# Performance work log

Hardware: AMD Instinct MI355X
Metric: run time of the kernel (lower is better)

The kernel has to match this reference:

```python
import jax, jax.numpy as jnp
import numpy as np


def setup_inputs() -> dict:
    key = jax.random.key(0)
    k1, k2 = jax.random.split(key)
    B, L, D = 32, 1024, 384
    MAX_LEN = 8192
    x = jax.random.normal(k1, (B, L, D), dtype=jnp.float32)
    # float durations in [0, 12); module rounds+clamps internally
    durations = jax.random.uniform(k2, (B, L), dtype=jnp.float32) * 12.0
    return {"x": x, "durations": durations, "max_len": MAX_LEN}


def reference(x, durations, max_len):
    # x: [B, L, D], durations: [B, L] (float), max_len: static python int
    B, L, D = x.shape
    dur = jnp.round(jnp.clip(durations, 0)).astype(jnp.int32)        # [B, L]
    cum = jnp.cumsum(dur, axis=1)                                    # [B, L] exclusive ends
    total = cum[:, -1]                                               # [B] expanded lengths
    t = jnp.arange(max_len, dtype=jnp.int32)                         # [T]
    # frame t belongs to phoneme idx where cum[idx-1] <= t < cum[idx]
    idx = jax.vmap(lambda c: jnp.searchsorted(c, t, side='right'))(cum)  # [B, T]
    idx = jnp.clip(idx, 0, L - 1)
    out = jnp.take_along_axis(x, idx[:, :, None], axis=1)            # [B, T, D]
    mask = (t[None, :] < total[:, None])[:, :, None]                 # [B, T, 1]
    return jnp.where(mask, out, jnp.zeros((), dtype=x.dtype))
```

## Files before the change

kernel.cpp:

```cpp
#include <hip/hip_runtime.h>
#include <hip/hip_bf16.h>


#define L_FIXED 1024
#define TILE_T 128
#define ROW_F4 96

__global__ __launch_bounds__(1024) void lr_cumsum_kernel(
    const float* __restrict__ durations, int* __restrict__ cum, int L) {
    __shared__ int s[L_FIXED];
    const int b = blockIdx.x;
    const int tid = threadIdx.x;
    float d = durations[b * L + tid];
    s[tid] = (int)rintf(fmaxf(d, 0.0f));
    __syncthreads();
#pragma unroll
    for (int off = 1; off < L_FIXED; off <<= 1) {
        int add = (tid >= off) ? s[tid - off] : 0;
        __syncthreads();
        s[tid] += add;
        __syncthreads();
    }
    cum[b * L + tid] = s[tid];
}

__global__ __launch_bounds__(256) void lr_gather_kernel(
    const float4* __restrict__ x, const int* __restrict__ cum,
    float4* __restrict__ out, int L, int max_len) {
    __shared__ int s_cum[L_FIXED];
    __shared__ int s_idx[TILE_T];
    const int b = blockIdx.y;
    const int t0 = blockIdx.x * TILE_T;
    const int tid = threadIdx.x;

    for (int i = tid; i < L; i += 256) s_cum[i] = cum[b * L + i];
    __syncthreads();

    const int total = s_cum[L - 1];
    if (tid < TILE_T) {
        const int t = t0 + tid;
        int lo = 0, hi = L;
        while (lo < hi) {
            int mid = (lo + hi) >> 1;
            if (s_cum[mid] <= t) lo = mid + 1; else hi = mid;
        }
        int idx = min(lo, L - 1);
        s_idx[tid] = (t < total) ? idx : -1;
    }
    __syncthreads();

    const long out_base = ((long)b * max_len + t0) * ROW_F4;
    const long x_base = (long)b * L * ROW_F4;
#pragma unroll
    for (int j = tid; j < TILE_T * ROW_F4; j += 256) {
        const int tl = j / ROW_F4;
        const int c = j - tl * ROW_F4;
        const int row = s_idx[tl];
        float4 v;
        if (row >= 0) {
            v = x[x_base + (long)row * ROW_F4 + c];
        } else {
            v = make_float4(0.f, 0.f, 0.f, 0.f);
        }
        out[out_base + (long)tl * ROW_F4 + c] = v;
    }
}

extern "C" void kernel_launch(void* const* d_in, const int* in_sizes, int n_in,
                              void* d_out, int out_size, void* d_ws, size_t ws_size,
                              hipStream_t stream) {
    const float* x = (const float*)d_in[0];
    const float* durations = (const float*)d_in[1];

    const int B = 32;
    const int L = 1024;
    const int MAX_LEN = 8192;

    int* cum = (int*)d_ws;

    lr_cumsum_kernel<<<B, L_FIXED, 0, stream>>>(durations, cum, L);

    dim3 grid(MAX_LEN / TILE_T, B);
    lr_gather_kernel<<<grid, 256, 0, stream>>>(
        (const float4*)x, cum, (float4*)d_out, L, MAX_LEN);
}
```

Measured before the change: 467.6 us.

## Move index search into scan kernel and use 2D row-copy gather blocks

The binary search from frame to phoneme now runs inside the per-batch scan kernel, which writes a precomputed index array to the workspace. The gather kernel then only loads 32 indices per block and copies rows with a 96x4 thread layout, so no integer division is needed. This removes the redundant per-block loading of the cumsum array and the search from the memory-bound copy. In exchange, the search now runs on only 32 blocks, which serialises it onto few CUs, and the copy grid becomes four times larger with smaller blocks.

```diff
diff --git a/kernel.cpp b/kernel.cpp
--- a/kernel.cpp
+++ b/kernel.cpp
@@ -2,67 +2,59 @@
 #include <hip/hip_bf16.h>
 
 
+#define B_FIXED 32
 #define L_FIXED 1024
-#define TILE_T 128
 #define ROW_F4 96
+#define RPB 32
 
-__global__ __launch_bounds__(1024) void lr_cumsum_kernel(
-    const float* __restrict__ durations, int* __restrict__ cum, int L) {
+__global__ __launch_bounds__(1024) void lr_scan_idx_kernel(
+    const float* __restrict__ durations, int* __restrict__ idx, int max_len) {
     __shared__ int s[L_FIXED];
     const int b = blockIdx.x;
     const int tid = threadIdx.x;
-    float d = durations[b * L + tid];
+    float d = durations[b * L_FIXED + tid];
     s[tid] = (int)rintf(fmaxf(d, 0.0f));
     __syncthreads();
-#pragma unroll
     for (int off = 1; off < L_FIXED; off <<= 1) {
         int add = (tid >= off) ? s[tid - off] : 0;
         __syncthreads();
         s[tid] += add;
         __syncthreads();
     }
-    cum[b * L + tid] = s[tid];
+    const int total = s[L_FIXED - 1];
+    for (int t = tid; t < max_len; t += 1024) {
+        int lo = 0, hi = L_FIXED;
+        while (lo < hi) {
+            int mid = (lo + hi) >> 1;
+            if (s[mid] <= t) lo = mid + 1; else hi = mid;
+        }
+        int v = min(lo, L_FIXED - 1);
+        idx[b * max_len + t] = (t < total) ? v : -1;
+    }
 }
 
-__global__ __launch_bounds__(256) void lr_gather_kernel(
-    const float4* __restrict__ x, const int* __restrict__ cum,
-    float4* __restrict__ out, int L, int max_len) {
-    __shared__ int s_cum[L_FIXED];
-    __shared__ int s_idx[TILE_T];
+__global__ __launch_bounds__(384) void lr_copy_kernel(
+    const float4* __restrict__ x, const int* __restrict__ idx,
+    float4* __restrict__ out, int max_len) {
+    __shared__ int s_idx[RPB];
     const int b = blockIdx.y;
-    const int t0 = blockIdx.x * TILE_T;
-    const int tid = threadIdx.x;
-
-    for (int i = tid; i < L; i += 256) s_cum[i] = cum[b * L + i];
+    const int t0 = blockIdx.x * RPB;
+    const int lin = threadIdx.y * 96 + threadIdx.x;
+    if (lin < RPB) s_idx[lin] = idx[b * max_len + t0 + lin];
     __syncthreads();
 
-    const int total = s_cum[L - 1];
-    if (tid < TILE_T) {
-        const int t = t0 + tid;
-        int lo = 0, hi = L;
-        while (lo < hi) {
-            int mid = (lo + hi) >> 1;
-            if (s_cum[mid] <= t) lo = mid + 1; else hi = mid;
-        }
-        int idx = min(lo, L - 1);
-        s_idx[tid] = (t < total) ? idx : -1;
-    }
-    __syncthreads();
-
-    const long out_base = ((long)b * max_len + t0) * ROW_F4;
-    const long x_base = (long)b * L * ROW_F4;
-#pragma unroll
-    for (int j = tid; j < TILE_T * ROW_F4; j += 256) {
-        const int tl = j / ROW_F4;
-        const int c = j - tl * ROW_F4;
-        const int row = s_idx[tl];
+    const long xbase = (long)b * L_FIXED * ROW_F4;
+    const long obase = ((long)b * max_len + t0) * ROW_F4;
+    const int cx = threadIdx.x;
+    for (int r = threadIdx.y; r < RPB; r += 4) {
+        const int row = s_idx[r];
         float4 v;
         if (row >= 0) {
-            v = x[x_base + (long)row * ROW_F4 + c];
+            v = x[xbase + (long)row * ROW_F4 + cx];
         } else {
             v = make_float4(0.f, 0.f, 0.f, 0.f);
         }
-        out[out_base + (long)tl * ROW_F4 + c] = v;
+        out[obase + (long)r * ROW_F4 + cx] = v;
     }
 }
 
@@ -71,16 +63,14 @@
                               hipStream_t stream) {
     const float* x = (const float*)d_in[0];
     const float* durations = (const float*)d_in[1];
-
-    const int B = 32;
-    const int L = 1024;
     const int MAX_LEN = 8192;
 
-    int* cum = (int*)d_ws;
+    int* idx = (int*)d_ws;
 
-    lr_cumsum_kernel<<<B, L_FIXED, 0, stream>>>(durations, cum, L);
+    lr_scan_idx_kernel<<<B_FIXED, 1024, 0, stream>>>(durations, idx, MAX_LEN);
 
-    dim3 grid(MAX_LEN / TILE_T, B);
-    lr_gather_kernel<<<grid, 256, 0, stream>>>(
-        (const float4*)x, cum, (float4*)d_out, L, MAX_LEN);
+    dim3 grid(MAX_LEN / RPB, B_FIXED);
+    dim3 block(96, 4);
+    lr_copy_kernel<<<grid, block, 0, stream>>>(
+        (const float4*)x, idx, (float4*)d_out, MAX_LEN);
 }
```

After: 454.2 us. 1.03x faster.
